# Performance work log

Measured on AMD Instinct MI355X. Metric: run time of the kernel, lower is better.

## Reference

```python
import jax, jax.numpy as jnp
import numpy as np

LOSS_WEIGHT = 1.0

def setup_inputs() -> dict:
    key = jax.random.key(0)
    k1, k2 = jax.random.split(key)
    point_set_1 = jax.random.normal(k1, (8, 4096, 2), dtype=jnp.float32)
    point_set_2 = jax.random.normal(k2, (8, 4096, 2), dtype=jnp.float32)
    return {"point_set_1": point_set_1, "point_set_2": point_set_2}

def reference(point_set_1, point_set_2):
    # Pairwise L2 distances: C[n, i, j] = ||x[n,i] - y[n,j]||_2  -> (N, P1, P2)
    diff = point_set_1[:, :, None, :] - point_set_2[:, None, :, :]
    C = jnp.sqrt(jnp.sum(diff * diff, axis=-1))
    d1 = jnp.min(C, axis=-1).mean(axis=-1)  # x -> nearest y
    d2 = jnp.min(C, axis=-2).mean(axis=-1)  # y -> nearest x
    dist = (d1 + d2) / 2.0                   # (N,)
    return dist * LOSS_WEIGHT
```

## Files before the change

kernel.cpp:

```cpp
#include <hip/hip_runtime.h>
#include <hip/hip_bf16.h>
#include <math.h>


#define B 8
#define N 4096
#define NJ 32
#define JC (N / NJ)
#define S1B 256
#define TX 16
#define NT 16
#define S2B 256

__global__ __launch_bounds__(S1B, 2) void chamfer_stage1(
    const float2* __restrict__ P1, const float2* __restrict__ P2,
    float* __restrict__ partial) {
  __shared__ float4 yb[JC];

  int b = blockIdx.x;
  int c = b % NJ; b /= NJ;
  int n = b % B;
  int dir = b / B;

  const float2* __restrict__ Q = dir ? P2 : P1;
  const float2* __restrict__ D = dir ? P1 : P2;

  const float2* dbase = D + n * N + c * JC;
  for (int t = threadIdx.x; t < JC; t += S1B) {
    float2 p = dbase[t];
    yb[t] = make_float4(-2.0f * p.x, -2.0f * p.y,
                        fmaf(p.x, p.x, p.y * p.y), 0.0f);
  }
  __syncthreads();

  float qx[TX], qy[TX], m[TX];
  const float2* qbase = Q + n * N + threadIdx.x;
#pragma unroll
  for (int k = 0; k < TX; ++k) {
    float2 q = qbase[k * S1B];
    qx[k] = q.x; qy[k] = q.y;
    m[k] = INFINITY;
  }

#pragma unroll 2
  for (int j = 0; j < JC; j += 2) {
    float4 y0 = yb[j];
    float4 y1 = yb[j + 1];
#pragma unroll
    for (int k = 0; k < TX; ++k) {
      float t0 = fmaf(qx[k], y0.x, fmaf(qy[k], y0.y, y0.z));
      float t1 = fmaf(qx[k], y1.x, fmaf(qy[k], y1.y, y1.z));
      asm("v_min3_f32 %0, %0, %1, %2" : "+v"(m[k]) : "v"(t0), "v"(t1));
    }
  }

  float* __restrict__ dst =
      partial + (((size_t)c * 2 + dir) * B + n) * N + threadIdx.x;
#pragma unroll
  for (int k = 0; k < TX; ++k) dst[k * S1B] = m[k];
}

__global__ __launch_bounds__(S2B) void chamfer_stage2(
    const float2* __restrict__ P1, const float2* __restrict__ P2,
    const float* __restrict__ partial, float* __restrict__ bs) {
  int b = blockIdx.x;
  int t = b % NT; b /= NT;
  int n = b % B;
  int dir = b / B;

  const float2* __restrict__ Q = dir ? P2 : P1;
  int i = t * S2B + threadIdx.x;

  float m = INFINITY;
  const float* __restrict__ pbase = partial + ((size_t)dir * B + n) * N + i;
#pragma unroll 8
  for (int c = 0; c < NJ; ++c)
    m = fminf(m, pbase[(size_t)c * 2 * B * N]);

  float2 q = Q[n * N + i];
  float d2 = m + fmaf(q.x, q.x, q.y * q.y);
  float sum = sqrtf(fmaxf(d2, 0.0f));

  __shared__ float red[S2B];
  red[threadIdx.x] = sum;
  __syncthreads();
  for (int s = S2B / 2; s > 0; s >>= 1) {
    if (threadIdx.x < s) red[threadIdx.x] += red[threadIdx.x + s];
    __syncthreads();
  }
  if (threadIdx.x == 0) bs[(dir * B + n) * NT + t] = red[0];
}

__global__ __launch_bounds__(64) void chamfer_stage3(
    const float* __restrict__ bs, float* __restrict__ out) {
  int n = blockIdx.x;
  int lane = threadIdx.x;
  float v = 0.0f;
  if (lane < 2 * NT) {
    int dir = lane / NT, t = lane % NT;
    v = bs[(dir * B + n) * NT + t];
  }
#pragma unroll
  for (int s = 32; s > 0; s >>= 1)
    v += __shfl_down(v, s, 64);
  if (lane == 0) out[n] = v * (0.5f / (float)N);
}

extern "C" void kernel_launch(void* const* d_in, const int* in_sizes, int n_in,
                              void* d_out, int out_size, void* d_ws, size_t ws_size,
                              hipStream_t stream) {
  const float2* P1 = (const float2*)d_in[0];
  const float2* P2 = (const float2*)d_in[1];
  float* out = (float*)d_out;
  float* partial = (float*)d_ws;
  float* bs = partial + (size_t)NJ * 2 * B * N;

  chamfer_stage1<<<dim3(2 * B * NJ), S1B, 0, stream>>>(P1, P2, partial);
  chamfer_stage2<<<dim3(2 * B * NT), S2B, 0, stream>>>(P1, P2, partial, bs);
  chamfer_stage3<<<dim3(B), 64, 0, stream>>>(bs, out);
}
```

Baseline: 35.14 us.

## Fuse final reduction into stage2 via atomic counter and retile stage1 grid

```diff
diff --git a/kernel.cpp b/kernel.cpp
--- a/kernel.cpp
+++ b/kernel.cpp
@@ -5,20 +5,26 @@
 
 #define B 8
 #define N 4096
-#define NJ 32
+#define NJ 16
+#define NI 2
+#define S1B 256
+#define TX 8
 #define JC (N / NJ)
-#define S1B 256
-#define TX 16
+#define JP (JC / 2)
 #define NT 16
 #define S2B 256
 
-__global__ __launch_bounds__(S1B, 2) void chamfer_stage1(
+__global__ __launch_bounds__(S1B) void chamfer_stage1(
     const float2* __restrict__ P1, const float2* __restrict__ P2,
-    float* __restrict__ partial) {
-  __shared__ float4 yb[JC];
+    float* __restrict__ partial, unsigned* __restrict__ cnt) {
+  __shared__ float4 axy[JP];
+  __shared__ float2 ssq[JP];
+
+  if (blockIdx.x == 0 && threadIdx.x < B) cnt[threadIdx.x] = 0;
 
   int b = blockIdx.x;
   int c = b % NJ; b /= NJ;
+  int itile = b % NI; b /= NI;
   int n = b % B;
   int dir = b / B;
 
@@ -26,15 +32,17 @@
   const float2* __restrict__ D = dir ? P1 : P2;
 
   const float2* dbase = D + n * N + c * JC;
-  for (int t = threadIdx.x; t < JC; t += S1B) {
-    float2 p = dbase[t];
-    yb[t] = make_float4(-2.0f * p.x, -2.0f * p.y,
-                        fmaf(p.x, p.x, p.y * p.y), 0.0f);
+  for (int t = threadIdx.x; t < JP; t += S1B) {
+    float2 p0 = dbase[2 * t];
+    float2 p1 = dbase[2 * t + 1];
+    axy[t] = make_float4(-2.f * p0.x, -2.f * p0.y, -2.f * p1.x, -2.f * p1.y);
+    ssq[t] = make_float2(fmaf(p0.x, p0.x, p0.y * p0.y),
+                         fmaf(p1.x, p1.x, p1.y * p1.y));
   }
   __syncthreads();
 
   float qx[TX], qy[TX], m[TX];
-  const float2* qbase = Q + n * N + threadIdx.x;
+  const float2* qbase = Q + n * N + itile * (S1B * TX) + threadIdx.x;
 #pragma unroll
   for (int k = 0; k < TX; ++k) {
     float2 q = qbase[k * S1B];
@@ -42,27 +50,28 @@
     m[k] = INFINITY;
   }
 
-#pragma unroll 2
-  for (int j = 0; j < JC; j += 2) {
-    float4 y0 = yb[j];
-    float4 y1 = yb[j + 1];
+#pragma unroll 4
+  for (int jp = 0; jp < JP; ++jp) {
+    float4 a = axy[jp];
+    float2 s = ssq[jp];
 #pragma unroll
     for (int k = 0; k < TX; ++k) {
-      float t0 = fmaf(qx[k], y0.x, fmaf(qy[k], y0.y, y0.z));
-      float t1 = fmaf(qx[k], y1.x, fmaf(qy[k], y1.y, y1.z));
-      asm("v_min3_f32 %0, %0, %1, %2" : "+v"(m[k]) : "v"(t0), "v"(t1));
+      float t0 = fmaf(qx[k], a.x, fmaf(qy[k], a.y, s.x));
+      float t1 = fmaf(qx[k], a.z, fmaf(qy[k], a.w, s.y));
+      m[k] = fminf(fminf(m[k], t0), t1);
     }
   }
 
-  float* __restrict__ dst =
-      partial + (((size_t)c * 2 + dir) * B + n) * N + threadIdx.x;
+  float* __restrict__ dst = partial + (((size_t)c * 2 + dir) * B + n) * N
+                          + itile * (S1B * TX) + threadIdx.x;
 #pragma unroll
   for (int k = 0; k < TX; ++k) dst[k * S1B] = m[k];
 }
 
 __global__ __launch_bounds__(S2B) void chamfer_stage2(
     const float2* __restrict__ P1, const float2* __restrict__ P2,
-    const float* __restrict__ partial, float* __restrict__ bs) {
+    const float* __restrict__ partial, float* __restrict__ bs,
+    unsigned* __restrict__ cnt, float* __restrict__ out) {
   int b = blockIdx.x;
   int t = b % NT; b /= NT;
   int n = b % B;
@@ -73,13 +82,12 @@
 
   float m = INFINITY;
   const float* __restrict__ pbase = partial + ((size_t)dir * B + n) * N + i;
-#pragma unroll 8
+#pragma unroll
   for (int c = 0; c < NJ; ++c)
     m = fminf(m, pbase[(size_t)c * 2 * B * N]);
 
   float2 q = Q[n * N + i];
-  float d2 = m + fmaf(q.x, q.x, q.y * q.y);
-  float sum = sqrtf(fmaxf(d2, 0.0f));
+  float sum = sqrtf(fmaxf(m + fmaf(q.x, q.x, q.y * q.y), 0.0f));
 
   __shared__ float red[S2B];
   red[threadIdx.x] = sum;
@@ -88,22 +96,29 @@
     if (threadIdx.x < s) red[threadIdx.x] += red[threadIdx.x + s];
     __syncthreads();
   }
-  if (threadIdx.x == 0) bs[(dir * B + n) * NT + t] = red[0];
-}
 
-__global__ __launch_bounds__(64) void chamfer_stage3(
-    const float* __restrict__ bs, float* __restrict__ out) {
-  int n = blockIdx.x;
-  int lane = threadIdx.x;
-  float v = 0.0f;
-  if (lane < 2 * NT) {
-    int dir = lane / NT, t = lane % NT;
-    v = bs[(dir * B + n) * NT + t];
+  __shared__ int last;
+  if (threadIdx.x == 0) {
+    bs[(dir * B + n) * NT + t] = red[0];
+    __threadfence();
+    unsigned r = atomicAdd(&cnt[n], 1u);
+    last = (r == 2 * NT - 1) ? 1 : 0;
   }
+  __syncthreads();
+
+  if (last && threadIdx.x < 64) {
+    float v = 0.0f;
+    if (threadIdx.x < 2 * NT) {
+      int dd = threadIdx.x / NT, tt = threadIdx.x % NT;
+      unsigned bits = atomicAdd(
+          (unsigned*)&bs[(dd * B + n) * NT + tt], 0u);
+      v = __uint_as_float(bits);
+    }
 #pragma unroll
-  for (int s = 32; s > 0; s >>= 1)
-    v += __shfl_down(v, s, 64);
-  if (lane == 0) out[n] = v * (0.5f / (float)N);
+    for (int s = 32; s > 0; s >>= 1)
+      v += __shfl_down(v, s, 64);
+    if (threadIdx.x == 0) out[n] = v * (0.5f / (float)N);
+  }
 }
 
 extern "C" void kernel_launch(void* const* d_in, const int* in_sizes, int n_in,
@@ -112,10 +127,11 @@
   const float2* P1 = (const float2*)d_in[0];
   const float2* P2 = (const float2*)d_in[1];
   float* out = (float*)d_out;
+
   float* partial = (float*)d_ws;
   float* bs = partial + (size_t)NJ * 2 * B * N;
+  unsigned* cnt = (unsigned*)(bs + 2 * B * NT);
 
-  chamfer_stage1<<<dim3(2 * B * NJ), S1B, 0, stream>>>(P1, P2, partial);
-  chamfer_stage2<<<dim3(2 * B * NT), S2B, 0, stream>>>(P1, P2, partial, bs);
-  chamfer_stage3<<<dim3(B), 64, 0, stream>>>(bs, out);
+  chamfer_stage1<<<dim3(2 * B * NI * NJ), S1B, 0, stream>>>(P1, P2, partial, cnt);
+  chamfer_stage2<<<dim3(2 * B * NT), S2B, 0, stream>>>(P1, P2, partial, bs, cnt, out);
 }
```

After: 31.33 us. 10.8% less time.
